# Kernel tuning notes

Measured on AMD Instinct MI355X. Metric: run time of the kernel, lower is better.

## Reference

```python
import jax, jax.numpy as jnp
import numpy as np

HID = 512      # hidden_size
IN = 1         # encoder/decoder input feature size
OUT = 1        # linear output size (feeds back as decoder input)
SEQ = 1000     # encoder sequence length
BATCH = 512
TGT = 1000     # target_len (decoder steps)


def setup_inputs() -> dict:
    key = jax.random.key(0)
    ks = jax.random.split(key, 11)
    s = 1.0 / np.sqrt(HID)  # PyTorch LSTM/Linear uniform init scale
    u = lambda k, shp: jax.random.uniform(k, shp, jnp.float32, -s, s)
    return {
        "input_batch": jax.random.normal(ks[0], (SEQ, BATCH, IN), jnp.float32),
        "enc_Wih": u(ks[1], (4 * HID, IN)),
        "enc_Whh": u(ks[2], (4 * HID, HID)),
        "enc_bih": u(ks[3], (4 * HID,)),
        "enc_bhh": u(ks[4], (4 * HID,)),
        "dec_Wih": u(ks[5], (4 * HID, OUT)),
        "dec_Whh": u(ks[6], (4 * HID, HID)),
        "dec_bih": u(ks[7], (4 * HID,)),
        "dec_bhh": u(ks[8], (4 * HID,)),
        "lin_W": u(ks[9], (OUT, HID)),
        "lin_b": u(ks[10], (OUT,)),
    }


def _lstm_cell(x, h, c, Wih, Whh, b):
    # PyTorch gate order: i, f, g, o
    gates = x @ Wih.T + h @ Whh.T + b  # [B, 4H]
    i, f, g, o = jnp.split(gates, 4, axis=-1)
    c = jax.nn.sigmoid(f) * c + jax.nn.sigmoid(i) * jnp.tanh(g)
    h = jax.nn.sigmoid(o) * jnp.tanh(c)
    return h, c


def reference(input_batch, enc_Wih, enc_Whh, enc_bih, enc_bhh,
              dec_Wih, dec_Whh, dec_bih, dec_bhh, lin_W, lin_b):
    batch = input_batch.shape[1]
    b_enc = enc_bih + enc_bhh
    b_dec = dec_bih + dec_bhh
    h0 = jnp.zeros((batch, HID), input_batch.dtype)

    # --- encoder: scan over SEQ time steps, zero initial state ---
    def enc_step(carry, x_t):
        h, c = carry
        h, c = _lstm_cell(x_t, h, c, enc_Wih, enc_Whh, b_enc)
        return (h, c), None

    (h, c), _ = jax.lax.scan(enc_step, (h0, h0), input_batch)

    x0 = jnp.zeros((batch, OUT), input_batch.dtype)

    def dec_step(carry, _):
        h, c, x = carry
        h, c = _lstm_cell(x, h, c, dec_Wih, dec_Whh, b_dec)
        pred = h @ lin_W.T + lin_b  # [B, OUT]
        return (h, c, pred), pred

    _, outputs = jax.lax.scan(dec_step, (h, c, x0), None, length=TGT)
    return outputs  # [TGT, BATCH, OUT]
```

## Files before the change

kernel.cpp:

```cpp
#include <hip/hip_runtime.h>


typedef _Float16 f16x8 __attribute__((ext_vector_type(8)));
typedef _Float16 f16x4 __attribute__((ext_vector_type(4)));
typedef float    f32x4 __attribute__((ext_vector_type(4)));
typedef unsigned long long u64;

#define GLOAD_LDS16(gp, lp)                                                    \
  __builtin_amdgcn_global_load_lds(                                            \
      (const __attribute__((address_space(1))) void*)(gp),                     \
      (__attribute__((address_space(3))) void*)(lp), 16, 0, 17)

__device__ __forceinline__ void store_h8_llc(_Float16* p, f16x4 v) {
  __hip_atomic_store((u64*)p, __builtin_bit_cast(u64, v),
                     __ATOMIC_RELAXED, __HIP_MEMORY_SCOPE_AGENT);
}

__device__ __forceinline__ float sigm(float x) {
  return __builtin_amdgcn_rcpf(1.0f + __expf(-x));
}
__device__ __forceinline__ float tanh_fast(float x) {
  float r = __expf(-2.0f*fabsf(x));
  float t = (1.0f - r)*__builtin_amdgcn_rcpf(1.0f + r);
  return copysignf(t, x);
}

__global__ void init_zero(float* __restrict__ out, int nout,
                          float* __restrict__ wsf, int nws) {
  int i = blockIdx.x*blockDim.x + threadIdx.x;
  int st = gridDim.x*blockDim.x;
  for (int j=i; j<nout; j+=st)
    __hip_atomic_store(&out[j], 0.f, __ATOMIC_RELAXED, __HIP_MEMORY_SCOPE_AGENT);
  for (int j=i; j<nws;  j+=st)
    __hip_atomic_store(&wsf[j], 0.f, __ATOMIC_RELAXED, __HIP_MEMORY_SCOPE_AGENT);
}

__global__ __launch_bounds__(256, 1) void lstm_main(
    const float* __restrict__ xin,
    const float* __restrict__ encWih, const float* __restrict__ encWhh,
    const float* __restrict__ enc_bih, const float* __restrict__ enc_bhh,
    const float* __restrict__ decWih, const float* __restrict__ decWhh,
    const float* __restrict__ dec_bih, const float* __restrict__ dec_bhh,
    const float* __restrict__ linW, const float* __restrict__ linb,
    float* __restrict__ out,
    _Float16* __restrict__ hbuf,
    int* __restrict__ flags)
{
  __shared__ f16x8 h_lds[4096];
  __shared__ float gates[64][68];

  const int bid = blockIdx.x, tid = threadIdx.x;
  const int rb = bid >> 5, hb = bid & 31;
  const int wid = tid >> 6, lane = tid & 63;
  const int wrow = wid >> 1, wcol = wid & 1;
  const int lcol = lane & 15, lq = lane >> 4, kq = lq*8;

  const int b_local = tid >> 2, u0 = (tid & 3)*4;
  const int bg = rb*64 + b_local;
  const int jh0 = hb*16 + u0;

  float linw[4];
  #pragma unroll
  for (int u=0; u<4; ++u) linw[u] = linW[jh0+u];
  const float linbv = linb[0];

  f16x8 wHi[2][16], wLo[2][16];
  float biasv[16], wihv[16];
  float c[4] = {0.f, 0.f, 0.f, 0.f};
  int* myflag = flags + (rb*32 + hb)*32;
  const int* pollp = flags + (rb*32 + (lane & 31))*32;

  int goff[16];
  #pragma unroll
  for (int i=0; i<16; ++i) {
    const int cch = i*256 + tid;
    const int pair = (cch >> 6) & 31;
    const int ks = pair >> 1, half = pair & 1;
    const int row_local = (cch >> 11)*32 + half*16 + lcol;
    goff[i] = row_local*512 + ks*32 + kq;
  }

  auto loadW = [&](const float* Whh, const float* bih, const float* bhh,
                   const float* Wih) {
    #pragma unroll
    for (int ct=0; ct<2; ++ct) {
      const int g = wcol*2 + ct;
      const float* wr = Whh + (size_t)(g*512 + hb*16 + lcol)*512;
      #pragma unroll
      for (int ks=0; ks<16; ++ks) {
        f16x8 hi, lo;
        #pragma unroll
        for (int i=0; i<8; ++i) {
          float w = wr[ks*32 + kq + i];
          _Float16 hh = (_Float16)w;
          float hf = (float)hh;
          float rem = (w - hf)*2048.0f;
          if (fabsf(hf) < 6.104e-5f) { hh = (_Float16)0.0f; rem = w*2048.0f; }
          hi[i] = hh; lo[i] = (_Float16)rem;
        }
        wHi[ct][ks] = hi; wLo[ct][ks] = lo;
      }
    }
    #pragma unroll
    for (int g=0; g<4; ++g)
      #pragma unroll
      for (int u=0; u<4; ++u) {
        int j = g*512 + jh0 + u;
        biasv[g*4+u] = bih[j] + bhh[j];
        wihv[g*4+u]  = Wih[j];
      }
  };

  loadW(encWhh, enc_bih, enc_bhh, encWih);

  for (int s=0; s<2000; ++s) {
    if (s == 1000) loadW(decWhh, dec_bih, dec_bhh, decWih);
    const bool dec = (s >= 1000);
    const int td = s - 1000;
    const _Float16* hr = hbuf + (size_t)((s+1)&1)*(512*512);
    _Float16*       hw = hbuf + (size_t)( s   &1)*(512*512);

    const _Float16* hrb = hr + (size_t)rb*64*512;
    f16x8* ldst = &h_lds[(size_t)wid*64];

    float x;
    if (!dec) x = xin[(size_t)s*512 + bg];
    else if (td == 0) x = 0.0f;
    else x = __hip_atomic_load(&out[(size_t)(td-1)*512 + bg],
                               __ATOMIC_RELAXED, __HIP_MEMORY_SCOPE_AGENT);

    #pragma unroll
    for (int i=0; i<16; ++i)
      GLOAD_LDS16(hrb + goff[i], ldst + i*256);
    __syncthreads();

    f32x4 accH[2][2], accL[2][2];
    #pragma unroll
    for (int rt=0; rt<2; ++rt)
      #pragma unroll
      for (int ctt=0; ctt<2; ++ctt) {
        accH[rt][ctt] = {0.f,0.f,0.f,0.f};
        accL[rt][ctt] = {0.f,0.f,0.f,0.f};
      }
    const f16x8* Ha = &h_lds[(size_t)wrow*2048];

    #pragma unroll
    for (int ks=0; ks<16; ++ks) {
      const f16x8 a0 = Ha[ks*128 + lane];
      const f16x8 a1 = Ha[ks*128 + 64 + lane];
      accH[0][0] = __builtin_amdgcn_mfma_f32_16x16x32_f16(a0, wHi[0][ks], accH[0][0], 0,0,0);
      accH[1][0] = __builtin_amdgcn_mfma_f32_16x16x32_f16(a1, wHi[0][ks], accH[1][0], 0,0,0);
      accH[0][1] = __builtin_amdgcn_mfma_f32_16x16x32_f16(a0, wHi[1][ks], accH[0][1], 0,0,0);
      accH[1][1] = __builtin_amdgcn_mfma_f32_16x16x32_f16(a1, wHi[1][ks], accH[1][1], 0,0,0);
      accL[0][0] = __builtin_amdgcn_mfma_f32_16x16x32_f16(a0, wLo[0][ks], accL[0][0], 0,0,0);
      accL[1][0] = __builtin_amdgcn_mfma_f32_16x16x32_f16(a1, wLo[0][ks], accL[1][0], 0,0,0);
      accL[0][1] = __builtin_amdgcn_mfma_f32_16x16x32_f16(a0, wLo[1][ks], accL[0][1], 0,0,0);
      accL[1][1] = __builtin_amdgcn_mfma_f32_16x16x32_f16(a1, wLo[1][ks], accL[1][1], 0,0,0);
    }

    #pragma unroll
    for (int rt=0; rt<2; ++rt)
      #pragma unroll
      for (int ctt=0; ctt<2; ++ctt) {
        f32x4 v = accH[rt][ctt] + accL[rt][ctt]*(1.0f/2048.0f);
        const int col  = wcol*32 + ctt*16 + lcol;
        const int row0 = wrow*32 + rt*16 + lq*4;
        #pragma unroll
        for (int i=0; i<4; ++i) gates[row0+i][col] = v[i];
      }
    __syncthreads();

    const f32x4 gi = *reinterpret_cast<const f32x4*>(&gates[b_local][ 0 + u0]);
    const f32x4 gf = *reinterpret_cast<const f32x4*>(&gates[b_local][16 + u0]);
    const f32x4 gg = *reinterpret_cast<const f32x4*>(&gates[b_local][32 + u0]);
    const f32x4 go = *reinterpret_cast<const f32x4*>(&gates[b_local][48 + u0]);

    f16x4 hv4;
    float sp = 0.f;
    #pragma unroll
    for (int u=0; u<4; ++u) {
      float ai = gi[u] + biasv[ 0+u] + x*wihv[ 0+u];
      float af = gf[u] + biasv[ 4+u] + x*wihv[ 4+u];
      float ag = gg[u] + biasv[ 8+u] + x*wihv[ 8+u];
      float ao = go[u] + biasv[12+u] + x*wihv[12+u];
      float iv = sigm(ai);
      float fv = sigm(af);
      float gv = tanh_fast(ag);
      float ov = sigm(ao);
      float cn = fv*c[u] + iv*gv;
      c[u] = cn;
      float hv = ov*tanh_fast(cn);
      hv4[u] = (_Float16)hv;
      sp += hv*linw[u];
    }
    store_h8_llc(hw + (size_t)bg*512 + jh0, hv4);

    if (dec) {
      sp += __shfl_xor(sp, 1);
      sp += __shfl_xor(sp, 2);
      if ((tid & 3) == 0) {
        float v = sp + (hb == 0 ? linbv : 0.f);
        __hip_atomic_fetch_add(&out[(size_t)td*512 + bg], v,
                               __ATOMIC_RELAXED, __HIP_MEMORY_SCOPE_AGENT);
      }
    }

    if (s != 1999) {
      asm volatile("s_waitcnt vmcnt(0)" ::: "memory");
      __syncthreads();
      const int av = s + 1;
      if (tid == 0)
        __hip_atomic_store(myflag, av, __ATOMIC_RELAXED, __HIP_MEMORY_SCOPE_AGENT);
      while (!__all(__hip_atomic_load(pollp, __ATOMIC_RELAXED,
                                      __HIP_MEMORY_SCOPE_AGENT) >= av)) { }
    }
  }
}

extern "C" void kernel_launch(void* const* d_in, const int* in_sizes, int n_in,
                              void* d_out, int out_size, void* d_ws, size_t ws_size,
                              hipStream_t stream) {
  const float* xin     = (const float*)d_in[0];
  const float* encWih  = (const float*)d_in[1];
  const float* encWhh  = (const float*)d_in[2];
  const float* enc_bih = (const float*)d_in[3];
  const float* enc_bhh = (const float*)d_in[4];
  const float* decWih  = (const float*)d_in[5];
  const float* decWhh  = (const float*)d_in[6];
  const float* dec_bih = (const float*)d_in[7];
  const float* dec_bhh = (const float*)d_in[8];
  const float* linW    = (const float*)d_in[9];
  const float* linb    = (const float*)d_in[10];
  float* out = (float*)d_out;
  char* ws = (char*)d_ws;
  int* flags = (int*)ws;
  _Float16* hbuf = (_Float16*)(ws + 32768);

  init_zero<<<512, 256, 0, stream>>>(out, 1000*512, (float*)ws,
                                     (32768 + 2*512*512*2)/4);

  lstm_main<<<dim3(256), dim3(256), 0, stream>>>(
      xin, encWih, encWhh, enc_bih, enc_bhh,
      decWih, decWhh, dec_bih, dec_bhh,
      linW, linb, out, hbuf, flags);
}
```

Baseline: 14.20 ms.

## Split batch rows across twice as many blocks, one gate per wave

```diff
diff --git a/kernel.cpp b/kernel.cpp
--- a/kernel.cpp
+++ b/kernel.cpp
@@ -2,17 +2,18 @@
 
 
 typedef _Float16 f16x8 __attribute__((ext_vector_type(8)));
-typedef _Float16 f16x4 __attribute__((ext_vector_type(4)));
+typedef _Float16 f16x2 __attribute__((ext_vector_type(2)));
 typedef float    f32x4 __attribute__((ext_vector_type(4)));
 typedef unsigned long long u64;
+typedef unsigned int u32;
 
 #define GLOAD_LDS16(gp, lp)                                                    \
   __builtin_amdgcn_global_load_lds(                                            \
       (const __attribute__((address_space(1))) void*)(gp),                     \
       (__attribute__((address_space(3))) void*)(lp), 16, 0, 17)
 
-__device__ __forceinline__ void store_h8_llc(_Float16* p, f16x4 v) {
-  __hip_atomic_store((u64*)p, __builtin_bit_cast(u64, v),
+__device__ __forceinline__ void store_h4_llc(_Float16* p, f16x2 v) {
+  __hip_atomic_store((u32*)p, __builtin_bit_cast(u32, v),
                      __ATOMIC_RELAXED, __HIP_MEMORY_SCOPE_AGENT);
 }
 
@@ -35,7 +36,7 @@
     __hip_atomic_store(&wsf[j], 0.f, __ATOMIC_RELAXED, __HIP_MEMORY_SCOPE_AGENT);
 }
 
-__global__ __launch_bounds__(256, 1) void lstm_main(
+__global__ __launch_bounds__(256, 2) void lstm_main(
     const float* __restrict__ xin,
     const float* __restrict__ encWih, const float* __restrict__ encWhh,
     const float* __restrict__ enc_bih, const float* __restrict__ enc_bhh,
@@ -46,68 +47,64 @@
     _Float16* __restrict__ hbuf,
     int* __restrict__ flags)
 {
-  __shared__ f16x8 h_lds[4096];
-  __shared__ float gates[64][68];
+  __shared__ f16x8 h_lds[2048];
+  __shared__ float gates[32][68];
 
   const int bid = blockIdx.x, tid = threadIdx.x;
   const int rb = bid >> 5, hb = bid & 31;
   const int wid = tid >> 6, lane = tid & 63;
-  const int wrow = wid >> 1, wcol = wid & 1;
   const int lcol = lane & 15, lq = lane >> 4, kq = lq*8;
 
-  const int b_local = tid >> 2, u0 = (tid & 3)*4;
-  const int bg = rb*64 + b_local;
+  const int b_local = tid >> 3, u0 = (tid & 7)*2;
+  const int bg = rb*32 + b_local;
   const int jh0 = hb*16 + u0;
 
-  float linw[4];
+  float linw[2];
   #pragma unroll
-  for (int u=0; u<4; ++u) linw[u] = linW[jh0+u];
+  for (int u=0; u<2; ++u) linw[u] = linW[jh0+u];
   const float linbv = linb[0];
 
-  f16x8 wHi[2][16], wLo[2][16];
-  float biasv[16], wihv[16];
-  float c[4] = {0.f, 0.f, 0.f, 0.f};
-  int* myflag = flags + (rb*32 + hb)*32;
+  f16x8 wHi[16], wLo[16];
+  float biasv[8], wihv[8];
+  float c[2] = {0.f, 0.f};
+  int* myflag = flags + bid*32;
   const int* pollp = flags + (rb*32 + (lane & 31))*32;
 
-  int goff[16];
+  int goff[8];
   #pragma unroll
-  for (int i=0; i<16; ++i) {
+  for (int i=0; i<8; ++i) {
     const int cch = i*256 + tid;
-    const int pair = (cch >> 6) & 31;
-    const int ks = pair >> 1, half = pair & 1;
-    const int row_local = (cch >> 11)*32 + half*16 + lcol;
-    goff[i] = row_local*512 + ks*32 + kq;
+    const int frag = cch >> 6;
+    const int ks = frag >> 1, half = frag & 1;
+    const int row_local = half*16 + (cch & 15);
+    goff[i] = row_local*512 + ks*32 + ((cch >> 4) & 3)*8;
   }
 
   auto loadW = [&](const float* Whh, const float* bih, const float* bhh,
                    const float* Wih) {
-    #pragma unroll
-    for (int ct=0; ct<2; ++ct) {
-      const int g = wcol*2 + ct;
-      const float* wr = Whh + (size_t)(g*512 + hb*16 + lcol)*512;
+    const int g = wid;
+    const float* wr = Whh + (size_t)(g*512 + hb*16 + lcol)*512;
+    #pragma unroll
+    for (int ks=0; ks<16; ++ks) {
+      f16x8 hi, lo;
       #pragma unroll
-      for (int ks=0; ks<16; ++ks) {
-        f16x8 hi, lo;
-        #pragma unroll
-        for (int i=0; i<8; ++i) {
-          float w = wr[ks*32 + kq + i];
-          _Float16 hh = (_Float16)w;
-          float hf = (float)hh;
-          float rem = (w - hf)*2048.0f;
-          if (fabsf(hf) < 6.104e-5f) { hh = (_Float16)0.0f; rem = w*2048.0f; }
-          hi[i] = hh; lo[i] = (_Float16)rem;
-        }
-        wHi[ct][ks] = hi; wLo[ct][ks] = lo;
-      }
-    }
-    #pragma unroll
-    for (int g=0; g<4; ++g)
+      for (int i=0; i<8; ++i) {
+        float w = wr[ks*32 + kq + i];
+        _Float16 hh = (_Float16)w;
+        float hf = (float)hh;
+        float rem = (w - hf)*2048.0f;
+        if (fabsf(hf) < 6.104e-5f) { hh = (_Float16)0.0f; rem = w*2048.0f; }
+        hi[i] = hh; lo[i] = (_Float16)rem;
+      }
+      wHi[ks] = hi; wLo[ks] = lo;
+    }
+    #pragma unroll
+    for (int gg=0; gg<4; ++gg)
       #pragma unroll
-      for (int u=0; u<4; ++u) {
-        int j = g*512 + jh0 + u;
-        biasv[g*4+u] = bih[j] + bhh[j];
-        wihv[g*4+u]  = Wih[j];
+      for (int u=0; u<2; ++u) {
+        int j = gg*512 + jh0 + u;
+        biasv[gg*2+u] = bih[j] + bhh[j];
+        wihv[gg*2+u]  = Wih[j];
       }
   };
 
@@ -120,7 +117,7 @@
     const _Float16* hr = hbuf + (size_t)((s+1)&1)*(512*512);
     _Float16*       hw = hbuf + (size_t)( s   &1)*(512*512);
 
-    const _Float16* hrb = hr + (size_t)rb*64*512;
+    const _Float16* hrb = hr + (size_t)rb*32*512;
     f16x8* ldst = &h_lds[(size_t)wid*64];
 
     float x;
@@ -130,59 +127,43 @@
                                __ATOMIC_RELAXED, __HIP_MEMORY_SCOPE_AGENT);
 
     #pragma unroll
-    for (int i=0; i<16; ++i)
+    for (int i=0; i<8; ++i)
       GLOAD_LDS16(hrb + goff[i], ldst + i*256);
     __syncthreads();
 
-    f32x4 accH[2][2], accL[2][2];
-    #pragma unroll
-    for (int rt=0; rt<2; ++rt)
+    f32x4 accH[2], accL[2];
+    accH[0] = {0.f,0.f,0.f,0.f}; accH[1] = {0.f,0.f,0.f,0.f};
+    accL[0] = {0.f,0.f,0.f,0.f}; accL[1] = {0.f,0.f,0.f,0.f};
+
+    #pragma unroll
+    for (int ks=0; ks<16; ++ks) {
+      const f16x8 a0 = h_lds[(ks*2+0)*64 + lane];
+      const f16x8 a1 = h_lds[(ks*2+1)*64 + lane];
+      accH[0] = __builtin_amdgcn_mfma_f32_16x16x32_f16(a0, wHi[ks], accH[0], 0,0,0);
+      accH[1] = __builtin_amdgcn_mfma_f32_16x16x32_f16(a1, wHi[ks], accH[1], 0,0,0);
+      accL[0] = __builtin_amdgcn_mfma_f32_16x16x32_f16(a0, wLo[ks], accL[0], 0,0,0);
+      accL[1] = __builtin_amdgcn_mfma_f32_16x16x32_f16(a1, wLo[ks], accL[1], 0,0,0);
+    }
+
+    #pragma unroll
+    for (int rt=0; rt<2; ++rt) {
+      f32x4 v = accH[rt] + accL[rt]*(1.0f/2048.0f);
+      const int col  = wid*16 + lcol;
+      const int row0 = rt*16 + lq*4;
       #pragma unroll
-      for (int ctt=0; ctt<2; ++ctt) {
-        accH[rt][ctt] = {0.f,0.f,0.f,0.f};
-        accL[rt][ctt] = {0.f,0.f,0.f,0.f};
-      }
-    const f16x8* Ha = &h_lds[(size_t)wrow*2048];
-
-    #pragma unroll
-    for (int ks=0; ks<16; ++ks) {
-      const f16x8 a0 = Ha[ks*128 + lane];
-      const f16x8 a1 = Ha[ks*128 + 64 + lane];
-      accH[0][0] = __builtin_amdgcn_mfma_f32_16x16x32_f16(a0, wHi[0][ks], accH[0][0], 0,0,0);
-      accH[1][0] = __builtin_amdgcn_mfma_f32_16x16x32_f16(a1, wHi[0][ks], accH[1][0], 0,0,0);
-      accH[0][1] = __builtin_amdgcn_mfma_f32_16x16x32_f16(a0, wHi[1][ks], accH[0][1], 0,0,0);
-      accH[1][1] = __builtin_amdgcn_mfma_f32_16x16x32_f16(a1, wHi[1][ks], accH[1][1], 0,0,0);
-      accL[0][0] = __builtin_amdgcn_mfma_f32_16x16x32_f16(a0, wLo[0][ks], accL[0][0], 0,0,0);
-      accL[1][0] = __builtin_amdgcn_mfma_f32_16x16x32_f16(a1, wLo[0][ks], accL[1][0], 0,0,0);
-      accL[0][1] = __builtin_amdgcn_mfma_f32_16x16x32_f16(a0, wLo[1][ks], accL[0][1], 0,0,0);
-      accL[1][1] = __builtin_amdgcn_mfma_f32_16x16x32_f16(a1, wLo[1][ks], accL[1][1], 0,0,0);
-    }
-
-    #pragma unroll
-    for (int rt=0; rt<2; ++rt)
-      #pragma unroll
-      for (int ctt=0; ctt<2; ++ctt) {
-        f32x4 v = accH[rt][ctt] + accL[rt][ctt]*(1.0f/2048.0f);
-        const int col  = wcol*32 + ctt*16 + lcol;
-        const int row0 = wrow*32 + rt*16 + lq*4;
-        #pragma unroll
-        for (int i=0; i<4; ++i) gates[row0+i][col] = v[i];
-      }
+      for (int i=0; i<4; ++i) gates[row0+i][col] = v[i];
+    }
     __syncthreads();
 
-    const f32x4 gi = *reinterpret_cast<const f32x4*>(&gates[b_local][ 0 + u0]);
-    const f32x4 gf = *reinterpret_cast<const f32x4*>(&gates[b_local][16 + u0]);
-    const f32x4 gg = *reinterpret_cast<const f32x4*>(&gates[b_local][32 + u0]);
-    const f32x4 go = *reinterpret_cast<const f32x4*>(&gates[b_local][48 + u0]);
-
-    f16x4 hv4;
+    const float* grow = gates[b_local];
+    f16x2 hv2;
     float sp = 0.f;
     #pragma unroll
-    for (int u=0; u<4; ++u) {
-      float ai = gi[u] + biasv[ 0+u] + x*wihv[ 0+u];
-      float af = gf[u] + biasv[ 4+u] + x*wihv[ 4+u];
-      float ag = gg[u] + biasv[ 8+u] + x*wihv[ 8+u];
-      float ao = go[u] + biasv[12+u] + x*wihv[12+u];
+    for (int u=0; u<2; ++u) {
+      float ai = grow[ 0 + u0+u] + biasv[0+u] + x*wihv[0+u];
+      float af = grow[16 + u0+u] + biasv[2+u] + x*wihv[2+u];
+      float ag = grow[32 + u0+u] + biasv[4+u] + x*wihv[4+u];
+      float ao = grow[48 + u0+u] + biasv[6+u] + x*wihv[6+u];
       float iv = sigm(ai);
       float fv = sigm(af);
       float gv = tanh_fast(ag);
@@ -190,15 +171,16 @@
       float cn = fv*c[u] + iv*gv;
       c[u] = cn;
       float hv = ov*tanh_fast(cn);
-      hv4[u] = (_Float16)hv;
+      hv2[u] = (_Float16)hv;
       sp += hv*linw[u];
     }
-    store_h8_llc(hw + (size_t)bg*512 + jh0, hv4);
+    store_h4_llc(hw + (size_t)bg*512 + jh0, hv2);
 
     if (dec) {
       sp += __shfl_xor(sp, 1);
       sp += __shfl_xor(sp, 2);
-      if ((tid & 3) == 0) {
+      sp += __shfl_xor(sp, 4);
+      if ((tid & 7) == 0) {
         float v = sp + (hb == 0 ? linbv : 0.f);
         __hip_atomic_fetch_add(&out[(size_t)td*512 + bg], v,
                                __ATOMIC_RELAXED, __HIP_MEMORY_SCOPE_AGENT);
@@ -211,8 +193,11 @@
       const int av = s + 1;
       if (tid == 0)
         __hip_atomic_store(myflag, av, __ATOMIC_RELAXED, __HIP_MEMORY_SCOPE_AGENT);
-      while (!__all(__hip_atomic_load(pollp, __ATOMIC_RELAXED,
-                                      __HIP_MEMORY_SCOPE_AGENT) >= av)) { }
+      if (wid == 0) {
+        while (!__all(__hip_atomic_load(pollp, __ATOMIC_RELAXED,
+                                        __HIP_MEMORY_SCOPE_AGENT) >= av)) { }
+      }
+      __syncthreads();
     }
   }
 }
@@ -234,12 +219,12 @@
   float* out = (float*)d_out;
   char* ws = (char*)d_ws;
   int* flags = (int*)ws;
-  _Float16* hbuf = (_Float16*)(ws + 32768);
+  _Float16* hbuf = (_Float16*)(ws + 65536);
 
   init_zero<<<512, 256, 0, stream>>>(out, 1000*512, (float*)ws,
-                                     (32768 + 2*512*512*2)/4);
-
-  lstm_main<<<dim3(256), dim3(256), 0, stream>>>(
+                                     (65536 + 2*512*512*2)/4);
+
+  lstm_main<<<dim3(512), dim3(256), 0, stream>>>(
       xin, encWih, encWhh, enc_bih, enc_bhh,
       decWih, decWhh, dec_bih, dec_bhh,
       linW, linb, out, hbuf, flags);
```

Result: faster. 12.53 ms (-11.8%).
